# Optimization experiments

Hardware: AMD Instinct MI355X
Metric: run time of the kernel (lower is better)

## Reference

```python
import jax, jax.numpy as jnp
import numpy as np

NUM_USERS = 100000
NUM_ITEMS = 50000
N_NODES = NUM_USERS + NUM_ITEMS
EMBED_DIM = 64
NUM_LAYERS = 3
NUM_EDGES = 1250000
EDGE_ATTR_DIM = 7
MLP_HID = 32
AUDIO_SCALE = 1.0
META_SCALE = 0.5


def _l2norm(x, eps=1e-12):
    # F.normalize(p=2, dim=-1): x / max(||x||, eps)
    n = jnp.sqrt(jnp.sum(x * x, axis=-1, keepdims=True))
    return x / jnp.maximum(n, eps)


def setup_inputs() -> dict:
    key = jax.random.key(0)
    ks = jax.random.split(key, 12)
    return {
        'user_emb_w': jax.random.normal(ks[0], (NUM_USERS, EMBED_DIM), jnp.float32),
        'artist_emb_w': jax.random.normal(ks[1], (20000, EMBED_DIM), jnp.float32),
        'album_emb_w': jax.random.normal(ks[2], (40000, EMBED_DIM), jnp.float32),
        'item_audio': jax.random.normal(ks[3], (NUM_ITEMS, EMBED_DIM), jnp.float32),
        'edge_attr': jax.random.normal(ks[4], (NUM_EDGES, EDGE_ATTR_DIM), jnp.float32),
        'edge_weight_init': jax.random.uniform(ks[5], (NUM_EDGES,), jnp.float32),
        'w1': jax.random.normal(ks[6], (EDGE_ATTR_DIM + 1, MLP_HID), jnp.float32),
        'b1': jnp.zeros((MLP_HID,), jnp.float32),
        'w2': jax.random.normal(ks[7], (MLP_HID, 1), jnp.float32),
        'b2': jnp.zeros((1,), jnp.float32),
        'edge_index': jax.random.randint(ks[8], (2, NUM_EDGES), 0, N_NODES, jnp.int64 if jax.config.read('jax_enable_x64') else jnp.int32),
        'artist_ids': jax.random.randint(ks[9], (NUM_ITEMS,), 0, 20000, jnp.int32),
        'album_ids': jax.random.randint(ks[10], (NUM_ITEMS,), 0, 40000, jnp.int32),
    }


def reference(user_emb_w, artist_emb_w, album_emb_w, item_audio, edge_attr,
              edge_weight_init, w1, b1, w2, b2, edge_index, artist_ids, album_ids):
    # Edge weight MLP: Linear -> ReLU -> Linear -> Sigmoid, squeezed
    ef = jnp.concatenate([edge_attr, edge_weight_init[:, None]], axis=1)  # [E, 8]
    h = jax.nn.relu(ef @ w1 + b1)
    w = jax.nn.sigmoid(h @ w2 + b2)[:, 0]  # [E]

    # Node features
    user_embed = _l2norm(user_emb_w)                                   # [U, D]
    meta = (artist_emb_w[artist_ids] + album_emb_w[album_ids]) * META_SCALE
    item_embed = _l2norm(item_audio * AUDIO_SCALE + meta)              # [I, D]
    x = jnp.concatenate([user_embed, item_embed], axis=0)              # [N, D]

    # gcn_norm (LGConv default, no self-loops): deg from target (col) scatter of w
    row, col = edge_index[0], edge_index[1]
    deg = jax.ops.segment_sum(w, col, num_segments=N_NODES)
    dinv = jnp.where(deg > 0, jax.lax.rsqrt(jnp.maximum(deg, 1e-30)), 0.0)
    norm = dinv[row] * w * dinv[col]                                   # [E]

    acc = x
    for _ in range(NUM_LAYERS):
        msg = norm[:, None] * x[row]                                   # [E, D]
        x = jax.ops.segment_sum(msg, col, num_segments=N_NODES)       # [N, D]
        acc = acc + x
    x = _l2norm(acc / (NUM_LAYERS + 1))

    user_emb = x[:NUM_USERS]
    item_emb = x[NUM_USERS:]
    align_loss = jnp.float32(0.0)
    return user_emb, item_emb, align_loss
```

## Files before the change

### kernel.cpp

```cpp
#include <hip/hip_runtime.h>
#include <hip/hip_bf16.h>
#include <math.h>

#define NUM_USERS  100000
#define NUM_ITEMS  50000
#define N_NODES    150000
#define EMBED_DIM  64
#define NUM_EDGES  1250000
#define MLP_HID    32
#define SCAN_B     1024
#define SCAN_NB    ((N_NODES + SCAN_B - 1) / SCAN_B)
#define NPW        4
#define PAD(x)     (((x) + 15) & ~15)

__global__ void hist_mlp(const float* __restrict__ edge_attr,
                         const float* __restrict__ ew,
                         const float* __restrict__ w1,
                         const float* __restrict__ b1,
                         const float* __restrict__ w2,
                         const float* __restrict__ b2,
                         const int*   __restrict__ edge_index,
                         int*   __restrict__ cnt,
                         int*   __restrict__ rank,
                         int2*  __restrict__ epair) {
    __shared__ float w1s[8 * MLP_HID];
    __shared__ float b1s[MLP_HID];
    __shared__ float w2s[MLP_HID];
    int tid = threadIdx.x;
    if (tid < 8 * MLP_HID) w1s[tid] = w1[tid];
    if (tid < MLP_HID) { b1s[tid] = b1[tid]; w2s[tid] = w2[tid]; }
    __syncthreads();

    int e = blockIdx.x * blockDim.x + tid;
    if (e >= NUM_EDGES) return;

    int c = edge_index[NUM_EDGES + e];
    rank[e] = atomicAdd(&cnt[c], 1);

    float ef[8];
#pragma unroll
    for (int k = 0; k < 7; ++k) ef[k] = edge_attr[e * 7 + k];
    ef[7] = ew[e];

    float s = b2[0];
#pragma unroll
    for (int j = 0; j < MLP_HID; ++j) {
        float h = b1s[j];
#pragma unroll
        for (int k = 0; k < 8; ++k) h = fmaf(ef[k], w1s[k * MLP_HID + j], h);
        h = fmaxf(h, 0.0f);
        s = fmaf(h, w2s[j], s);
    }
    float w = 1.0f / (1.0f + expf(-s));

    int2 pr;
    pr.x = edge_index[e];
    pr.y = __float_as_int(w);
    epair[e] = pr;
}

__global__ void scan_partial(const int* __restrict__ cnt,
                             int* __restrict__ part) {
    __shared__ int s[SCAN_B];
    int tid = threadIdx.x;
    int i = blockIdx.x * SCAN_B + tid;
    s[tid] = (i < N_NODES) ? PAD(cnt[i]) : 0;
    __syncthreads();
#pragma unroll
    for (int off = SCAN_B / 2; off > 0; off >>= 1) {
        if (tid < off) s[tid] += s[tid + off];
        __syncthreads();
    }
    if (tid == 0) part[blockIdx.x] = s[0];
}

__global__ void scan_offsets(const int* __restrict__ part,
                             int* __restrict__ base_off) {
    __shared__ int s[256];
    int tid = threadIdx.x;
    int v = (tid < SCAN_NB) ? part[tid] : 0;
    s[tid] = v;
    __syncthreads();
#pragma unroll
    for (int off = 1; off < 256; off <<= 1) {
        int t = (tid >= off) ? s[tid - off] : 0;
        __syncthreads();
        s[tid] += t;
        __syncthreads();
    }
    if (tid < SCAN_NB) base_off[tid] = s[tid] - v;
}

__global__ void scan_apply(const int* __restrict__ cnt,
                           const int* __restrict__ base_off,
                           int* __restrict__ row_ptr) {
    __shared__ int s[SCAN_B];
    int tid = threadIdx.x;
    int i = blockIdx.x * SCAN_B + tid;
    int v = (i < N_NODES) ? PAD(cnt[i]) : 0;
    s[tid] = v;
    __syncthreads();
    for (int off = 1; off < SCAN_B; off <<= 1) {
        int t = (tid >= off) ? s[tid - off] : 0;
        __syncthreads();
        s[tid] += t;
        __syncthreads();
    }
    if (i < N_NODES) row_ptr[i] = s[tid] - v + base_off[blockIdx.x];
    if (i == N_NODES - 1) row_ptr[N_NODES] = s[tid] + base_off[blockIdx.x];
}

__global__ void scatter_perm(const int* __restrict__ edge_index,
                             const int* __restrict__ rank,
                             const int* __restrict__ row_ptr,
                             int* __restrict__ perm) {
    int t = blockIdx.x * blockDim.x + threadIdx.x;
    int e = 4 * t;
    if (e >= NUM_EDGES) return;
#pragma unroll
    for (int q = 0; q < 4; ++q) {
        int c = edge_index[NUM_EDGES + e + q];
        perm[row_ptr[c] + rank[e + q]] = e + q;
    }
}

__global__ void pair_build(const int* __restrict__ row_ptr,
                           const int* __restrict__ cnt,
                           const int* __restrict__ perm,
                           const int2* __restrict__ epair,
                           int2* __restrict__ csr_pair,
                           float* __restrict__ dinv,
                           float* __restrict__ dinv2,
                           float* __restrict__ rd) {
    int t = blockIdx.x * blockDim.x + threadIdx.x;
    int node = t >> 4;
    int lane = t & 15;
    if (node >= N_NODES) return;
    int s = row_ptr[node];
    int e = row_ptr[node + 1];
    int re = s + cnt[node];
    float sum = 0.0f;
    for (int j = s + lane; j < e; j += 16) {
        int2 pr;
        if (j < re) {
            int eid = perm[j];
            pr = epair[eid];
            sum += __int_as_float(pr.y);
        } else {
            pr.x = 0; pr.y = 0;
        }
        csr_pair[j] = pr;
    }
    sum += __shfl_xor(sum, 8);
    sum += __shfl_xor(sum, 4);
    sum += __shfl_xor(sum, 2);
    sum += __shfl_xor(sum, 1);
    if (lane == 0) {
        float dv = (sum > 0.0f) ? rsqrtf(fmaxf(sum, 1e-30f)) : 0.0f;
        dinv[node]  = dv;
        dinv2[node] = dv * dv;
        rd[node]    = (dv > 0.0f) ? (1.0f / dv) : 0.0f;
    }
    if (node == N_NODES - 1) {
        int2 z; z.x = 0; z.y = 0;
        for (int q = lane; q < 64; q += 16) csr_pair[e + q] = z;
    }
}

__global__ void init_x(const float* __restrict__ user_w,
                       const float* __restrict__ artist_w,
                       const float* __restrict__ album_w,
                       const float* __restrict__ audio,
                       const int*   __restrict__ artist_ids,
                       const int*   __restrict__ album_ids,
                       const float* __restrict__ dinv,
                       float* __restrict__ x0out,
                       unsigned short* __restrict__ y0) {
    int t = blockIdx.x * blockDim.x + threadIdx.x;
    int row = t >> 6;
    int lane = t & 63;
    if (row >= N_NODES) return;

    float v;
    if (row < NUM_USERS) {
        v = user_w[row * EMBED_DIM + lane];
    } else {
        int r = row - NUM_USERS;
        int ar = artist_ids[r];
        int al = album_ids[r];
        v = audio[r * EMBED_DIM + lane]
          + 0.5f * (artist_w[ar * EMBED_DIM + lane] + album_w[al * EMBED_DIM + lane]);
    }
    float ss = v * v;
#pragma unroll
    for (int off = 32; off > 0; off >>= 1) ss += __shfl_xor(ss, off);
    float scale = 1.0f / fmaxf(sqrtf(ss), 1e-12f);
    float x0 = v * scale;
    size_t o = (size_t)row * EMBED_DIM + lane;
    x0out[o] = x0;
    y0[o] = __bfloat16_as_ushort(__float2bfloat16(x0 * dinv[row]));
}

#define BF_LO(u) __uint_as_float((u) << 16)
#define BF_HI(u) __uint_as_float((u) & 0xffff0000u)

__global__ void propagate_mid(const int* __restrict__ row_ptr,
                              const int2* __restrict__ csr_pair,
                              const float* __restrict__ dinv2,
                              const unsigned short* __restrict__ yin,
                              unsigned short* __restrict__ yout) {
    int wave = (blockIdx.x * blockDim.x + threadIdx.x) >> 6;
    int lane = threadIdx.x & 63;
    int node0 = wave * NPW;
    if (node0 >= N_NODES) return;

    int eg = lane >> 4;
    int dq = (lane & 15) << 2;

    int rpv = row_ptr[node0 + (lane <= NPW ? lane : NPW)];
    int rs0 = __shfl(rpv, 0);
    int rs1 = __shfl(rpv, 1);
    int rs2 = __shfl(rpv, 2);
    int rs3 = __shfl(rpv, 3);
    int rs4 = __shfl(rpv, 4);

    int j = rs0 + (eg << 2);
    int2 pa0 = csr_pair[j];
    int2 pa1 = csr_pair[j + 1];
    int2 pa2 = csr_pair[j + 2];
    int2 pa3 = csr_pair[j + 3];

#pragma unroll
    for (int k = 0; k < NPW; ++k) {
        int bs = (k == 0) ? rs0 : (k == 1) ? rs1 : (k == 2) ? rs2 : rs3;
        int be = (k == 0) ? rs1 : (k == 1) ? rs2 : (k == 2) ? rs3 : rs4;
        float a0 = 0, a1 = 0, a2 = 0, a3 = 0;

        for (int base = bs; base < be; base += 16) {
            int   s0 = pa0.x; float w0 = __int_as_float(pa0.y);
            int   s1 = pa1.x; float w1 = __int_as_float(pa1.y);
            int   s2 = pa2.x; float w2 = __int_as_float(pa2.y);
            int   s3 = pa3.x; float w3 = __int_as_float(pa3.y);

            uint2 u0 = *(const uint2*)(yin + ((size_t)s0 << 6) + dq);
            uint2 u1 = *(const uint2*)(yin + ((size_t)s1 << 6) + dq);
            uint2 u2 = *(const uint2*)(yin + ((size_t)s2 << 6) + dq);
            uint2 u3 = *(const uint2*)(yin + ((size_t)s3 << 6) + dq);

            j += 16;
            pa0 = csr_pair[j];
            pa1 = csr_pair[j + 1];
            pa2 = csr_pair[j + 2];
            pa3 = csr_pair[j + 3];

            a0 = fmaf(w0, BF_LO(u0.x), a0); a1 = fmaf(w0, BF_HI(u0.x), a1);
            a2 = fmaf(w0, BF_LO(u0.y), a2); a3 = fmaf(w0, BF_HI(u0.y), a3);
            a0 = fmaf(w1, BF_LO(u1.x), a0); a1 = fmaf(w1, BF_HI(u1.x), a1);
            a2 = fmaf(w1, BF_LO(u1.y), a2); a3 = fmaf(w1, BF_HI(u1.y), a3);
            a0 = fmaf(w2, BF_LO(u2.x), a0); a1 = fmaf(w2, BF_HI(u2.x), a1);
            a2 = fmaf(w2, BF_LO(u2.y), a2); a3 = fmaf(w2, BF_HI(u2.y), a3);
            a0 = fmaf(w3, BF_LO(u3.x), a0); a1 = fmaf(w3, BF_HI(u3.x), a1);
            a2 = fmaf(w3, BF_LO(u3.y), a2); a3 = fmaf(w3, BF_HI(u3.y), a3);
        }

        a0 += __shfl_xor(a0, 16); a1 += __shfl_xor(a1, 16);
        a2 += __shfl_xor(a2, 16); a3 += __shfl_xor(a3, 16);
        a0 += __shfl_xor(a0, 32); a1 += __shfl_xor(a1, 32);
        a2 += __shfl_xor(a2, 32); a3 += __shfl_xor(a3, 32);

        if (eg == 0) {
            float dc2 = dinv2[node0 + k];
            size_t o = ((size_t)(node0 + k) << 6) + dq;
            unsigned int b0 = (unsigned int)__bfloat16_as_ushort(__float2bfloat16(a0 * dc2));
            unsigned int b1 = (unsigned int)__bfloat16_as_ushort(__float2bfloat16(a1 * dc2));
            unsigned int b2 = (unsigned int)__bfloat16_as_ushort(__float2bfloat16(a2 * dc2));
            unsigned int b3 = (unsigned int)__bfloat16_as_ushort(__float2bfloat16(a3 * dc2));
            uint2 u;
            u.x = b0 | (b1 << 16);
            u.y = b2 | (b3 << 16);
            *(uint2*)(yout + o) = u;
        }
    }
}

__global__ void propagate_final(const int* __restrict__ row_ptr,
                                const int2* __restrict__ csr_pair,
                                const float* __restrict__ dinv,
                                const float* __restrict__ rd,
                                const unsigned short* __restrict__ y1,
                                const unsigned short* __restrict__ y2,
                                float* __restrict__ outp) {
    int wave = (blockIdx.x * blockDim.x + threadIdx.x) >> 6;
    int lane = threadIdx.x & 63;
    int node0 = wave * NPW;
    if (node0 >= N_NODES) return;

    int eg = lane >> 4;
    int dq = (lane & 15) << 2;

    int rpv = row_ptr[node0 + (lane <= NPW ? lane : NPW)];
    int rs0 = __shfl(rpv, 0);
    int rs1 = __shfl(rpv, 1);
    int rs2 = __shfl(rpv, 2);
    int rs3 = __shfl(rpv, 3);
    int rs4 = __shfl(rpv, 4);

    int j = rs0 + (eg << 2);
    int2 pa0 = csr_pair[j];
    int2 pa1 = csr_pair[j + 1];
    int2 pa2 = csr_pair[j + 2];
    int2 pa3 = csr_pair[j + 3];

#pragma unroll
    for (int k = 0; k < NPW; ++k) {
        int bs = (k == 0) ? rs0 : (k == 1) ? rs1 : (k == 2) ? rs2 : rs3;
        int be = (k == 0) ? rs1 : (k == 1) ? rs2 : (k == 2) ? rs3 : rs4;
        float a0 = 0, a1 = 0, a2 = 0, a3 = 0;

        for (int base = bs; base < be; base += 16) {
            int   s0 = pa0.x; float w0 = __int_as_float(pa0.y);
            int   s1 = pa1.x; float w1 = __int_as_float(pa1.y);
            int   s2 = pa2.x; float w2 = __int_as_float(pa2.y);
            int   s3 = pa3.x; float w3 = __int_as_float(pa3.y);

            uint2 u0 = *(const uint2*)(y2 + ((size_t)s0 << 6) + dq);
            uint2 u1 = *(const uint2*)(y2 + ((size_t)s1 << 6) + dq);
            uint2 u2 = *(const uint2*)(y2 + ((size_t)s2 << 6) + dq);
            uint2 u3 = *(const uint2*)(y2 + ((size_t)s3 << 6) + dq);

            j += 16;
            pa0 = csr_pair[j];
            pa1 = csr_pair[j + 1];
            pa2 = csr_pair[j + 2];
            pa3 = csr_pair[j + 3];

            a0 = fmaf(w0, BF_LO(u0.x), a0); a1 = fmaf(w0, BF_HI(u0.x), a1);
            a2 = fmaf(w0, BF_LO(u0.y), a2); a3 = fmaf(w0, BF_HI(u0.y), a3);
            a0 = fmaf(w1, BF_LO(u1.x), a0); a1 = fmaf(w1, BF_HI(u1.x), a1);
            a2 = fmaf(w1, BF_LO(u1.y), a2); a3 = fmaf(w1, BF_HI(u1.y), a3);
            a0 = fmaf(w2, BF_LO(u2.x), a0); a1 = fmaf(w2, BF_HI(u2.x), a1);
            a2 = fmaf(w2, BF_LO(u2.y), a2); a3 = fmaf(w2, BF_HI(u2.y), a3);
            a0 = fmaf(w3, BF_LO(u3.x), a0); a1 = fmaf(w3, BF_HI(u3.x), a1);
            a2 = fmaf(w3, BF_LO(u3.y), a2); a3 = fmaf(w3, BF_HI(u3.y), a3);
        }

        a0 += __shfl_xor(a0, 16); a1 += __shfl_xor(a1, 16);
        a2 += __shfl_xor(a2, 16); a3 += __shfl_xor(a3, 16);
        a0 += __shfl_xor(a0, 32); a1 += __shfl_xor(a1, 32);
        a2 += __shfl_xor(a2, 32); a3 += __shfl_xor(a3, 32);

        if (eg == 0) {
            int node = node0 + k;
            float dv  = dinv[node];
            float rdv = rd[node];
            size_t o = ((size_t)node << 6) + dq;
            float4 x0v = *(const float4*)(outp + o);
            uint2 u1v = *(const uint2*)(y1 + o);
            uint2 u2v = *(const uint2*)(y2 + o);

            float v0 = (x0v.x + rdv * (BF_LO(u1v.x) + BF_LO(u2v.x)) + dv * a0) * 0.25f;
            float v1 = (x0v.y + rdv * (BF_HI(u1v.x) + BF_HI(u2v.x)) + dv * a1) * 0.25f;
            float v2 = (x0v.z + rdv * (BF_LO(u1v.y) + BF_LO(u2v.y)) + dv * a2) * 0.25f;
            float v3 = (x0v.w + rdv * (BF_HI(u1v.y) + BF_HI(u2v.y)) + dv * a3) * 0.25f;

            float ss = v0 * v0 + v1 * v1 + v2 * v2 + v3 * v3;
            ss += __shfl_xor(ss, 1);
            ss += __shfl_xor(ss, 2);
            ss += __shfl_xor(ss, 4);
            ss += __shfl_xor(ss, 8);
            float scale = 1.0f / fmaxf(sqrtf(ss), 1e-12f);

            float4 r = { v0 * scale, v1 * scale, v2 * scale, v3 * scale };
            *(float4*)(outp + o) = r;
        }
    }
    if (blockIdx.x == 0 && threadIdx.x == 0)
        outp[(size_t)N_NODES * EMBED_DIM] = 0.0f;
}

#undef BF_LO
#undef BF_HI

extern "C" void kernel_launch(void* const* d_in, const int* in_sizes, int n_in,
                              void* d_out, int out_size, void* d_ws, size_t ws_size,
                              hipStream_t stream) {
    const float* user_w     = (const float*)d_in[0];
    const float* artist_w   = (const float*)d_in[1];
    const float* album_w    = (const float*)d_in[2];
    const float* audio      = (const float*)d_in[3];
    const float* edge_attr  = (const float*)d_in[4];
    const float* ew         = (const float*)d_in[5];
    const float* w1         = (const float*)d_in[6];
    const float* b1         = (const float*)d_in[7];
    const float* w2         = (const float*)d_in[8];
    const float* b2         = (const float*)d_in[9];
    const int*   edge_index = (const int*)d_in[10];
    const int*   artist_ids = (const int*)d_in[11];
    const int*   album_ids  = (const int*)d_in[12];
    float* out = (float*)d_out;

    float* ws = (float*)d_ws;
    unsigned short* y0 = (unsigned short*)ws;
    unsigned short* y1 = (unsigned short*)(ws + 4800000);
    unsigned short* y2 = (unsigned short*)(ws + 9600000);
    float* dinv    = ws + 14400000;
    float* dinv2   = ws + 14560000;
    float* rd      = ws + 14720000;
    int*  row_ptr  = (int*)(ws + 14880000);
    int2* csr_pair = (int2*)(ws + 15040000);
    int*   cnt     = (int*)ws;
    int*   rank    = (int*)(ws + 150000);
    int*   part    = (int*)(ws + 1600000);
    int*   baseoff = (int*)(ws + 1601000);
    int2*  epair   = (int2*)(ws + 1700000);
    int*   perm    = (int*)(ws + 4800000);

    const int B = 256;
    const int egrid   = (NUM_EDGES + B - 1) / B;
    const int egrid4  = (NUM_EDGES / 4 + B - 1) / B;
    const int ngrid   = (N_NODES * EMBED_DIM) / B;
    const int ngrid16 = (N_NODES * 16) / B;
    const int pgrid   = (N_NODES / NPW * 64) / B;

    hipMemsetAsync(cnt, 0, N_NODES * sizeof(int), stream);

    hist_mlp<<<egrid, B, 0, stream>>>(
        edge_attr, ew, w1, b1, w2, b2, edge_index, cnt, rank, epair);

    scan_partial<<<SCAN_NB, SCAN_B, 0, stream>>>(cnt, part);
    scan_offsets<<<1, 256, 0, stream>>>(part, baseoff);
    scan_apply<<<SCAN_NB, SCAN_B, 0, stream>>>(cnt, baseoff, row_ptr);

    scatter_perm<<<egrid4, B, 0, stream>>>(edge_index, rank, row_ptr, perm);

    pair_build<<<ngrid16, B, 0, stream>>>(
        row_ptr, cnt, perm, epair, csr_pair, dinv, dinv2, rd);

    init_x<<<ngrid, B, 0, stream>>>(
        user_w, artist_w, album_w, audio, artist_ids, album_ids,
        dinv, out, y0);

    propagate_mid<<<pgrid, B, 0, stream>>>(row_ptr, csr_pair, dinv2, y0, y1);
    propagate_mid<<<pgrid, B, 0, stream>>>(row_ptr, csr_pair, dinv2, y1, y2);
    propagate_final<<<pgrid, B, 0, stream>>>(row_ptr, csr_pair, dinv, rd, y1, y2, out);
}
```

Before: 401.0 us.

## Build CSR by direct atomic scatter of MLP results, dropping rank/perm passes

The CSR build changes shape. A lightweight count pass now does the histogram, and the edge MLP runs after the scan, writing each (row, weight) pair straight into its CSR slot through an atomic write pointer. This removes the separate rank array, the perm scatter, the epair buffer and the indirect gather in pair_build. The cost is a second atomic pass over the edges and a nondeterministic order of edges within each row, which can change the floating-point summation order.

```diff
diff --git a/kernel.cpp b/kernel.cpp
--- a/kernel.cpp
+++ b/kernel.cpp
@@ -13,50 +13,16 @@
 #define NPW        4
 #define PAD(x)     (((x) + 15) & ~15)
 
-__global__ void hist_mlp(const float* __restrict__ edge_attr,
-                         const float* __restrict__ ew,
-                         const float* __restrict__ w1,
-                         const float* __restrict__ b1,
-                         const float* __restrict__ w2,
-                         const float* __restrict__ b2,
-                         const int*   __restrict__ edge_index,
-                         int*   __restrict__ cnt,
-                         int*   __restrict__ rank,
-                         int2*  __restrict__ epair) {
-    __shared__ float w1s[8 * MLP_HID];
-    __shared__ float b1s[MLP_HID];
-    __shared__ float w2s[MLP_HID];
-    int tid = threadIdx.x;
-    if (tid < 8 * MLP_HID) w1s[tid] = w1[tid];
-    if (tid < MLP_HID) { b1s[tid] = b1[tid]; w2s[tid] = w2[tid]; }
-    __syncthreads();
-
-    int e = blockIdx.x * blockDim.x + tid;
+__global__ void count4(const int* __restrict__ edge_index,
+                       int* __restrict__ cnt) {
+    int t = blockIdx.x * blockDim.x + threadIdx.x;
+    int e = 4 * t;
     if (e >= NUM_EDGES) return;
-
-    int c = edge_index[NUM_EDGES + e];
-    rank[e] = atomicAdd(&cnt[c], 1);
-
-    float ef[8];
-#pragma unroll
-    for (int k = 0; k < 7; ++k) ef[k] = edge_attr[e * 7 + k];
-    ef[7] = ew[e];
-
-    float s = b2[0];
-#pragma unroll
-    for (int j = 0; j < MLP_HID; ++j) {
-        float h = b1s[j];
-#pragma unroll
-        for (int k = 0; k < 8; ++k) h = fmaf(ef[k], w1s[k * MLP_HID + j], h);
-        h = fmaxf(h, 0.0f);
-        s = fmaf(h, w2s[j], s);
-    }
-    float w = 1.0f / (1.0f + expf(-s));
-
-    int2 pr;
-    pr.x = edge_index[e];
-    pr.y = __float_as_int(w);
-    epair[e] = pr;
+    int4 c = *(const int4*)(edge_index + NUM_EDGES + e);
+    atomicAdd(&cnt[c.x], 1);
+    atomicAdd(&cnt[c.y], 1);
+    atomicAdd(&cnt[c.z], 1);
+    atomicAdd(&cnt[c.w], 1);
 }
 
 __global__ void scan_partial(const int* __restrict__ cnt,
@@ -93,7 +59,8 @@
 
 __global__ void scan_apply(const int* __restrict__ cnt,
                            const int* __restrict__ base_off,
-                           int* __restrict__ row_ptr) {
+                           int* __restrict__ row_ptr,
+                           int* __restrict__ wp) {
     __shared__ int s[SCAN_B];
     int tid = threadIdx.x;
     int i = blockIdx.x * SCAN_B + tid;
@@ -106,51 +73,77 @@
         s[tid] += t;
         __syncthreads();
     }
-    if (i < N_NODES) row_ptr[i] = s[tid] - v + base_off[blockIdx.x];
+    if (i < N_NODES) {
+        int v0 = s[tid] - v + base_off[blockIdx.x];
+        row_ptr[i] = v0;
+        wp[i] = v0;
+    }
     if (i == N_NODES - 1) row_ptr[N_NODES] = s[tid] + base_off[blockIdx.x];
 }
 
-__global__ void scatter_perm(const int* __restrict__ edge_index,
-                             const int* __restrict__ rank,
-                             const int* __restrict__ row_ptr,
-                             int* __restrict__ perm) {
-    int t = blockIdx.x * blockDim.x + threadIdx.x;
-    int e = 4 * t;
+__global__ void mlp_scatter(const float* __restrict__ edge_attr,
+                            const float* __restrict__ ew,
+                            const float* __restrict__ w1,
+                            const float* __restrict__ b1,
+                            const float* __restrict__ w2,
+                            const float* __restrict__ b2,
+                            const int*   __restrict__ edge_index,
+                            int*  __restrict__ wp,
+                            int2* __restrict__ csr_pair) {
+    __shared__ float w1s[8 * MLP_HID];
+    __shared__ float b1s[MLP_HID];
+    __shared__ float w2s[MLP_HID];
+    int tid = threadIdx.x;
+    if (tid < 8 * MLP_HID) w1s[tid] = w1[tid];
+    if (tid < MLP_HID) { b1s[tid] = b1[tid]; w2s[tid] = w2[tid]; }
+    __syncthreads();
+
+    int e = blockIdx.x * blockDim.x + tid;
     if (e >= NUM_EDGES) return;
-#pragma unroll
-    for (int q = 0; q < 4; ++q) {
-        int c = edge_index[NUM_EDGES + e + q];
-        perm[row_ptr[c] + rank[e + q]] = e + q;
-    }
-}
-
-__global__ void pair_build(const int* __restrict__ row_ptr,
-                           const int* __restrict__ cnt,
-                           const int* __restrict__ perm,
-                           const int2* __restrict__ epair,
-                           int2* __restrict__ csr_pair,
-                           float* __restrict__ dinv,
-                           float* __restrict__ dinv2,
-                           float* __restrict__ rd) {
+
+    int c = edge_index[NUM_EDGES + e];
+    int pos = atomicAdd(&wp[c], 1);
+
+    float ef[8];
+#pragma unroll
+    for (int k = 0; k < 7; ++k) ef[k] = edge_attr[e * 7 + k];
+    ef[7] = ew[e];
+
+    float s = b2[0];
+#pragma unroll
+    for (int j = 0; j < MLP_HID; ++j) {
+        float h = b1s[j];
+#pragma unroll
+        for (int k = 0; k < 8; ++k) h = fmaf(ef[k], w1s[k * MLP_HID + j], h);
+        h = fmaxf(h, 0.0f);
+        s = fmaf(h, w2s[j], s);
+    }
+    float w = 1.0f / (1.0f + expf(-s));
+
+    int2 pr;
+    pr.x = edge_index[e];
+    pr.y = __float_as_int(w);
+    csr_pair[pos] = pr;
+}
+
+__global__ void degpad(const int* __restrict__ row_ptr,
+                       const int* __restrict__ cnt,
+                       int2* __restrict__ csr_pair,
+                       float* __restrict__ dinv,
+                       float* __restrict__ dinv2,
+                       float* __restrict__ rd) {
     int t = blockIdx.x * blockDim.x + threadIdx.x;
     int node = t >> 4;
     int lane = t & 15;
     if (node >= N_NODES) return;
-    int s = row_ptr[node];
-    int e = row_ptr[node + 1];
+    int s  = row_ptr[node];
+    int e  = row_ptr[node + 1];
     int re = s + cnt[node];
     float sum = 0.0f;
-    for (int j = s + lane; j < e; j += 16) {
-        int2 pr;
-        if (j < re) {
-            int eid = perm[j];
-            pr = epair[eid];
-            sum += __int_as_float(pr.y);
-        } else {
-            pr.x = 0; pr.y = 0;
-        }
-        csr_pair[j] = pr;
-    }
+    for (int j = s + lane; j < re; j += 16)
+        sum += __int_as_float(csr_pair[j].y);
+    int2 z; z.x = 0; z.y = 0;
+    for (int j = re + lane; j < e; j += 16) csr_pair[j] = z;
     sum += __shfl_xor(sum, 8);
     sum += __shfl_xor(sum, 4);
     sum += __shfl_xor(sum, 2);
@@ -162,7 +155,6 @@
         rd[node]    = (dv > 0.0f) ? (1.0f / dv) : 0.0f;
     }
     if (node == N_NODES - 1) {
-        int2 z; z.x = 0; z.y = 0;
         for (int q = lane; q < 64; q += 16) csr_pair[e + q] = z;
     }
 }
@@ -407,13 +399,11 @@
     float* dinv2   = ws + 14560000;
     float* rd      = ws + 14720000;
     int*  row_ptr  = (int*)(ws + 14880000);
-    int2* csr_pair = (int2*)(ws + 15040000);
+    int*  wp       = (int*)(ws + 15040000);
+    int2* csr_pair = (int2*)(ws + 15200000);
     int*   cnt     = (int*)ws;
-    int*   rank    = (int*)(ws + 150000);
-    int*   part    = (int*)(ws + 1600000);
-    int*   baseoff = (int*)(ws + 1601000);
-    int2*  epair   = (int2*)(ws + 1700000);
-    int*   perm    = (int*)(ws + 4800000);
+    int*   part    = (int*)(ws + 200000);
+    int*   baseoff = (int*)(ws + 201000);
 
     const int B = 256;
     const int egrid   = (NUM_EDGES + B - 1) / B;
@@ -424,17 +414,17 @@
 
     hipMemsetAsync(cnt, 0, N_NODES * sizeof(int), stream);
 
-    hist_mlp<<<egrid, B, 0, stream>>>(
-        edge_attr, ew, w1, b1, w2, b2, edge_index, cnt, rank, epair);
+    count4<<<egrid4, B, 0, stream>>>(edge_index, cnt);
 
     scan_partial<<<SCAN_NB, SCAN_B, 0, stream>>>(cnt, part);
     scan_offsets<<<1, 256, 0, stream>>>(part, baseoff);
-    scan_apply<<<SCAN_NB, SCAN_B, 0, stream>>>(cnt, baseoff, row_ptr);
-
-    scatter_perm<<<egrid4, B, 0, stream>>>(edge_index, rank, row_ptr, perm);
-
-    pair_build<<<ngrid16, B, 0, stream>>>(
-        row_ptr, cnt, perm, epair, csr_pair, dinv, dinv2, rd);
+    scan_apply<<<SCAN_NB, SCAN_B, 0, stream>>>(cnt, baseoff, row_ptr, wp);
+
+    mlp_scatter<<<egrid, B, 0, stream>>>(
+        edge_attr, ew, w1, b1, w2, b2, edge_index, wp, csr_pair);
+
+    degpad<<<ngrid16, B, 0, stream>>>(
+        row_ptr, cnt, csr_pair, dinv, dinv2, rd);
 
     init_x<<<ngrid, B, 0, stream>>>(
         user_w, artist_w, album_w, audio, artist_ids, album_ids,
```

Result: slower. 432.3 us (+7.8%).

## Shard degree histogram atomics eightfold and fuse pair build with embedding init

Applied to the files above, without the earlier changes.

The histogram atomics are split across 8 copies selected by block index, which reduces contention on hot target nodes. A new reduce8 kernel turns the per-copy counts into exclusive prefixes and totals, and scatter_perm reads the copy prefix to place each edge, now using vectorized int4 loads. The CSR pair build is fused with x0 initialization (float4 per 16-lane group), which removes one launch and one read of dinv. The costs are a larger memset (8x N counters), an extra reduction kernel, and a workspace layout that changes where buffers sit.

```diff
diff --git a/kernel.cpp b/kernel.cpp
--- a/kernel.cpp
+++ b/kernel.cpp
@@ -20,7 +20,7 @@
                          const float* __restrict__ w2,
                          const float* __restrict__ b2,
                          const int*   __restrict__ edge_index,
-                         int*   __restrict__ cnt,
+                         int*   __restrict__ cnt8,
                          int*   __restrict__ rank,
                          int2*  __restrict__ epair) {
     __shared__ float w1s[8 * MLP_HID];
@@ -34,8 +34,9 @@
     int e = blockIdx.x * blockDim.x + tid;
     if (e >= NUM_EDGES) return;
 
+    int sh = blockIdx.x & 7;
     int c = edge_index[NUM_EDGES + e];
-    rank[e] = atomicAdd(&cnt[c], 1);
+    int lr = atomicAdd(&cnt8[sh * N_NODES + c], 1);
 
     float ef[8];
 #pragma unroll
@@ -53,10 +54,25 @@
     }
     float w = 1.0f / (1.0f + expf(-s));
 
+    rank[e] = lr | (sh << 28);
     int2 pr;
     pr.x = edge_index[e];
     pr.y = __float_as_int(w);
     epair[e] = pr;
+}
+
+__global__ void reduce8(int* __restrict__ cnt8,
+                        int* __restrict__ cnt) {
+    int n = blockIdx.x * blockDim.x + threadIdx.x;
+    if (n >= N_NODES) return;
+    int acc = 0;
+#pragma unroll
+    for (int s = 0; s < 8; ++s) {
+        int c = cnt8[s * N_NODES + n];
+        cnt8[s * N_NODES + n] = acc;
+        acc += c;
+    }
+    cnt[n] = acc;
 }
 
 __global__ void scan_partial(const int* __restrict__ cnt,
@@ -113,25 +129,41 @@
 __global__ void scatter_perm(const int* __restrict__ edge_index,
                              const int* __restrict__ rank,
                              const int* __restrict__ row_ptr,
+                             const int* __restrict__ cnt8,
                              int* __restrict__ perm) {
     int t = blockIdx.x * blockDim.x + threadIdx.x;
     int e = 4 * t;
     if (e >= NUM_EDGES) return;
+    int4 cc = *(const int4*)(edge_index + NUM_EDGES + e);
+    int4 rr = *(const int4*)(rank + e);
+    int cs[4] = { cc.x, cc.y, cc.z, cc.w };
+    int rs[4] = { rr.x, rr.y, rr.z, rr.w };
 #pragma unroll
     for (int q = 0; q < 4; ++q) {
-        int c = edge_index[NUM_EDGES + e + q];
-        perm[row_ptr[c] + rank[e + q]] = e + q;
-    }
-}
-
-__global__ void pair_build(const int* __restrict__ row_ptr,
-                           const int* __restrict__ cnt,
-                           const int* __restrict__ perm,
-                           const int2* __restrict__ epair,
-                           int2* __restrict__ csr_pair,
-                           float* __restrict__ dinv,
-                           float* __restrict__ dinv2,
-                           float* __restrict__ rd) {
+        int c  = cs[q];
+        int sh = rs[q] >> 28;
+        int lr = rs[q] & 0x0FFFFFFF;
+        int pref = cnt8[sh * N_NODES + c];
+        perm[row_ptr[c] + pref + lr] = e + q;
+    }
+}
+
+__global__ void pair_build_init(const int* __restrict__ row_ptr,
+                                const int* __restrict__ cnt,
+                                const int* __restrict__ perm,
+                                const int2* __restrict__ epair,
+                                const float* __restrict__ user_w,
+                                const float* __restrict__ artist_w,
+                                const float* __restrict__ album_w,
+                                const float* __restrict__ audio,
+                                const int*   __restrict__ artist_ids,
+                                const int*   __restrict__ album_ids,
+                                int2* __restrict__ csr_pair,
+                                float* __restrict__ dinv,
+                                float* __restrict__ dinv2,
+                                float* __restrict__ rd,
+                                float* __restrict__ x0out,
+                                unsigned short* __restrict__ y0) {
     int t = blockIdx.x * blockDim.x + threadIdx.x;
     int node = t >> 4;
     int lane = t & 15;
@@ -139,6 +171,7 @@
     int s = row_ptr[node];
     int e = row_ptr[node + 1];
     int re = s + cnt[node];
+
     float sum = 0.0f;
     for (int j = s + lane; j < e; j += 16) {
         int2 pr;
@@ -155,8 +188,8 @@
     sum += __shfl_xor(sum, 4);
     sum += __shfl_xor(sum, 2);
     sum += __shfl_xor(sum, 1);
+    float dv = (sum > 0.0f) ? rsqrtf(fmaxf(sum, 1e-30f)) : 0.0f;
     if (lane == 0) {
-        float dv = (sum > 0.0f) ? rsqrtf(fmaxf(sum, 1e-30f)) : 0.0f;
         dinv[node]  = dv;
         dinv2[node] = dv * dv;
         rd[node]    = (dv > 0.0f) ? (1.0f / dv) : 0.0f;
@@ -165,40 +198,41 @@
         int2 z; z.x = 0; z.y = 0;
         for (int q = lane; q < 64; q += 16) csr_pair[e + q] = z;
     }
-}
-
-__global__ void init_x(const float* __restrict__ user_w,
-                       const float* __restrict__ artist_w,
-                       const float* __restrict__ album_w,
-                       const float* __restrict__ audio,
-                       const int*   __restrict__ artist_ids,
-                       const int*   __restrict__ album_ids,
-                       const float* __restrict__ dinv,
-                       float* __restrict__ x0out,
-                       unsigned short* __restrict__ y0) {
-    int t = blockIdx.x * blockDim.x + threadIdx.x;
-    int row = t >> 6;
-    int lane = t & 63;
-    if (row >= N_NODES) return;
-
-    float v;
-    if (row < NUM_USERS) {
-        v = user_w[row * EMBED_DIM + lane];
+
+    float4 v;
+    if (node < NUM_USERS) {
+        v = *(const float4*)(user_w + (size_t)node * EMBED_DIM + lane * 4);
     } else {
-        int r = row - NUM_USERS;
+        int r = node - NUM_USERS;
         int ar = artist_ids[r];
         int al = album_ids[r];
-        v = audio[r * EMBED_DIM + lane]
-          + 0.5f * (artist_w[ar * EMBED_DIM + lane] + album_w[al * EMBED_DIM + lane]);
-    }
-    float ss = v * v;
-#pragma unroll
-    for (int off = 32; off > 0; off >>= 1) ss += __shfl_xor(ss, off);
+        float4 a  = *(const float4*)(audio    + (size_t)r  * EMBED_DIM + lane * 4);
+        float4 b  = *(const float4*)(artist_w + (size_t)ar * EMBED_DIM + lane * 4);
+        float4 cl = *(const float4*)(album_w  + (size_t)al * EMBED_DIM + lane * 4);
+        v.x = a.x + 0.5f * (b.x + cl.x);
+        v.y = a.y + 0.5f * (b.y + cl.y);
+        v.z = a.z + 0.5f * (b.z + cl.z);
+        v.w = a.w + 0.5f * (b.w + cl.w);
+    }
+    float ss = v.x * v.x + v.y * v.y + v.z * v.z + v.w * v.w;
+    ss += __shfl_xor(ss, 1);
+    ss += __shfl_xor(ss, 2);
+    ss += __shfl_xor(ss, 4);
+    ss += __shfl_xor(ss, 8);
     float scale = 1.0f / fmaxf(sqrtf(ss), 1e-12f);
-    float x0 = v * scale;
-    size_t o = (size_t)row * EMBED_DIM + lane;
-    x0out[o] = x0;
-    y0[o] = __bfloat16_as_ushort(__float2bfloat16(x0 * dinv[row]));
+    float4 x0;
+    x0.x = v.x * scale; x0.y = v.y * scale;
+    x0.z = v.z * scale; x0.w = v.w * scale;
+    size_t o = ((size_t)node << 6) + lane * 4;
+    *(float4*)(x0out + o) = x0;
+    unsigned int b0 = (unsigned int)__bfloat16_as_ushort(__float2bfloat16(x0.x * dv));
+    unsigned int b1 = (unsigned int)__bfloat16_as_ushort(__float2bfloat16(x0.y * dv));
+    unsigned int b2 = (unsigned int)__bfloat16_as_ushort(__float2bfloat16(x0.z * dv));
+    unsigned int b3 = (unsigned int)__bfloat16_as_ushort(__float2bfloat16(x0.w * dv));
+    uint2 u;
+    u.x = b0 | (b1 << 16);
+    u.y = b2 | (b3 << 16);
+    *(uint2*)(y0 + o) = u;
 }
 
 #define BF_LO(u) __uint_as_float((u) << 16)
@@ -407,38 +441,40 @@
     float* dinv2   = ws + 14560000;
     float* rd      = ws + 14720000;
     int*  row_ptr  = (int*)(ws + 14880000);
-    int2* csr_pair = (int2*)(ws + 15040000);
-    int*   cnt     = (int*)ws;
-    int*   rank    = (int*)(ws + 150000);
-    int*   part    = (int*)(ws + 1600000);
-    int*   baseoff = (int*)(ws + 1601000);
-    int2*  epair   = (int2*)(ws + 1700000);
-    int*   perm    = (int*)(ws + 4800000);
+    int*  cnt      = (int*)(ws + 15040000);
+    int*  cnt8     = (int*)(ws + 15200000);
+    int*  part     = (int*)(ws + 16450000);
+    int*  baseoff  = (int*)(ws + 16451000);
+    int2* csr_pair = (int2*)(ws + 16500000);
+    int2* epair = (int2*)(ws + 4800000);
+    int*  rank  = (int*)(ws + 9600000);
+    int*  perm  = (int*)(ws + 10850000);
 
     const int B = 256;
     const int egrid   = (NUM_EDGES + B - 1) / B;
     const int egrid4  = (NUM_EDGES / 4 + B - 1) / B;
-    const int ngrid   = (N_NODES * EMBED_DIM) / B;
     const int ngrid16 = (N_NODES * 16) / B;
+    const int dgrid   = (N_NODES + B - 1) / B;
     const int pgrid   = (N_NODES / NPW * 64) / B;
 
-    hipMemsetAsync(cnt, 0, N_NODES * sizeof(int), stream);
+    hipMemsetAsync(cnt8, 0, 8 * N_NODES * sizeof(int), stream);
 
     hist_mlp<<<egrid, B, 0, stream>>>(
-        edge_attr, ew, w1, b1, w2, b2, edge_index, cnt, rank, epair);
+        edge_attr, ew, w1, b1, w2, b2, edge_index, cnt8, rank, epair);
+
+    reduce8<<<dgrid, B, 0, stream>>>(cnt8, cnt);
 
     scan_partial<<<SCAN_NB, SCAN_B, 0, stream>>>(cnt, part);
     scan_offsets<<<1, 256, 0, stream>>>(part, baseoff);
     scan_apply<<<SCAN_NB, SCAN_B, 0, stream>>>(cnt, baseoff, row_ptr);
 
-    scatter_perm<<<egrid4, B, 0, stream>>>(edge_index, rank, row_ptr, perm);
-
-    pair_build<<<ngrid16, B, 0, stream>>>(
-        row_ptr, cnt, perm, epair, csr_pair, dinv, dinv2, rd);
-
-    init_x<<<ngrid, B, 0, stream>>>(
+    scatter_perm<<<egrid4, B, 0, stream>>>(
+        edge_index, rank, row_ptr, cnt8, perm);
+
+    pair_build_init<<<ngrid16, B, 0, stream>>>(
+        row_ptr, cnt, perm, epair,
         user_w, artist_w, album_w, audio, artist_ids, album_ids,
-        dinv, out, y0);
+        csr_pair, dinv, dinv2, rd, out, y0);
 
     propagate_mid<<<pgrid, B, 0, stream>>>(row_ptr, csr_pair, dinv2, y0, y1);
     propagate_mid<<<pgrid, B, 0, stream>>>(row_ptr, csr_pair, dinv2, y1, y2);
```

Result: faster. 389.7 us (-2.8%).
